# Kernel tuning notes

Measured on AMD Instinct MI355X. Metric: run time of the kernel, lower is better.

## Reference

```python
import jax, jax.numpy as jnp
import numpy as np

B, M, D, HK = 1024, 40, 64, 128

def setup_inputs() -> dict:
    key = jax.random.key(0)
    k1, k2, k3, k4 = jax.random.split(key, 4)
    scale0 = (2.0 / (M + HK)) ** 0.5  # glorot-ish
    scale = (2.0 / (HK + HK)) ** 0.5
    return {
        "x": jax.random.normal(k1, (B, M, D), dtype=jnp.float32),
        "W0": jax.random.normal(k2, (M, M, HK), dtype=jnp.float32) * scale0,
        "W1": jax.random.normal(k3, (M, HK, HK), dtype=jnp.float32) * scale,
        "W2": jax.random.normal(k4, (M, HK, HK), dtype=jnp.float32) * scale,
    }

def reference(x, W0, W1, W2):
    # x: [B, m, D]; layer i: x_next[b,h,d] = sum_{i,j} x0[b,i,d]*xk[b,j,d]*W[i,j,h]
    x0 = x
    xk = x
    outs = []
    for W in (W0, W1, W2):
        # pairwise field interactions per embedding dim: [B, D, m, Hprev]
        z = jnp.einsum('bid,bjd->bdij', x0, xk)
        # contract over both field axes with the filter: [B, Hk, D]
        xk = jnp.einsum('bdij,ijh->bhd', z, W)
        # sum-pool over embedding dim: [B, Hk]
        outs.append(jnp.sum(xk, axis=2))
    return jnp.concatenate(outs, axis=1)  # [B, Hk*k]
```

## Files before the change

### kernel.cpp

```cpp
#include <hip/hip_runtime.h>
#include <cstdint>
#include <cstddef>


typedef __attribute__((ext_vector_type(4))) float f4v;
typedef __attribute__((ext_vector_type(8))) short s8v;

__device__ __forceinline__ unsigned short f2bf(float f){
  unsigned u = __float_as_uint(f);
  u += 0x7fffu + ((u >> 16) & 1u);
  return (unsigned short)(u >> 16);
}

__global__ void prep_weights(const float* __restrict__ W0,
                             const float* __restrict__ W1,
                             const float* __restrict__ W2,
                             unsigned short* __restrict__ ws)
{
  const int total = 327680 + 655360 + 655360;
  for (int e = blockIdx.x * blockDim.x + threadIdx.x; e < total;
       e += gridDim.x * blockDim.x){
    float w; int hi, lo;
    if (e < 327680){
      int h = e / 2560, k = e % 2560;
      int i = k >> 6, j = k & 63;
      w = (j < 40) ? W0[(i*40 + j)*128 + h] : 0.f;
      hi = e; lo = 327680 + e;
    } else if (e < 983040){
      int r = e - 327680;
      int h = r / 5120, k = r % 5120;
      w = W1[k*128 + h];
      hi = 655360 + r; lo = 1310720 + r;
    } else {
      int r = e - 983040;
      int h = r / 5120, k = r % 5120;
      w = W2[k*128 + h];
      hi = 1966080 + r; lo = 2621440 + r;
    }
    unsigned short hb = f2bf(w);
    float whf = __uint_as_float((unsigned)hb << 16);
    unsigned short lb = f2bf(w - whf);
    ws[hi] = hb; ws[lo] = lb;
  }
}


template<int J, int KT>
__device__ __forceinline__ void run_layer(
    const unsigned short* __restrict__ Whi,
    const unsigned short* __restrict__ Wlo,
    const float* __restrict__ xg,
    float* xk, float* __restrict__ out,
    int layerOff, int blockRow, int tid)
{
  const int lane = tid & 63;
  const int wv   = tid >> 6;
  const int cgi  = wv & 1, rgi = wv >> 1;
  const int lrow = lane & 15, q = lane >> 4;

  f4v acc[4][4];
#pragma unroll
  for (int a = 0; a < 4; a++)
#pragma unroll
    for (int b = 0; b < 4; b++)
      acc[a][b] = (f4v){0.f, 0.f, 0.f, 0.f};

  const unsigned short* wp[4];
  const unsigned short* wq[4];
#pragma unroll
  for (int nt = 0; nt < 4; nt++){
    int col = cgi*64 + nt*16 + lrow;
    wp[nt] = Whi + (size_t)col * KT + q*8;
    wq[nt] = Wlo + (size_t)col * KT + q*8;
  }

#pragma unroll 1
  for (int i = 0; i < 40; i++){
    float x0[4];
#pragma unroll
    for (int rt = 0; rt < 4; rt++){
      int gr = blockRow + rgi*64 + rt*16 + lrow;
      x0[rt] = xg[((gr >> 6)*40 + i)*64 + (gr & 63)];
    }
#pragma unroll
    for (int jb = 0; jb < J/32; jb++){
      const int k0 = i*J + jb*32;
      s8v bh[4], bl[4];
#pragma unroll
      for (int nt = 0; nt < 4; nt++){
        bh[nt] = *(const s8v*)(wp[nt] + k0);
        bl[nt] = *(const s8v*)(wq[nt] + k0);
      }
#pragma unroll
      for (int rt = 0; rt < 4; rt++){
        int row = rgi*64 + rt*16 + lrow;
        int w0 = row*128 + ((jb*32 + q*8) ^ ((row & 7) << 2));
        f4v v0 = *(const f4v*)(xk + w0);
        f4v v1 = *(const f4v*)(xk + (w0 ^ 4));
        float s = x0[rt];
        float a0 = s*v0[0], a1 = s*v0[1], a2 = s*v0[2], a3 = s*v0[3];
        float a4 = s*v1[0], a5 = s*v1[1], a6 = s*v1[2], a7 = s*v1[3];
        unsigned ah01, ah23, ah45, ah67, al01, al23, al45, al67;
        asm("v_cvt_pk_bf16_f32 %0, %1, %2" : "=v"(ah01) : "v"(a0), "v"(a1));
        asm("v_cvt_pk_bf16_f32 %0, %1, %2" : "=v"(ah23) : "v"(a2), "v"(a3));
        asm("v_cvt_pk_bf16_f32 %0, %1, %2" : "=v"(ah45) : "v"(a4), "v"(a5));
        asm("v_cvt_pk_bf16_f32 %0, %1, %2" : "=v"(ah67) : "v"(a6), "v"(a7));
        float r0 = a0 - __uint_as_float(ah01 << 16);
        float r1 = a1 - __uint_as_float(ah01 & 0xffff0000u);
        float r2 = a2 - __uint_as_float(ah23 << 16);
        float r3 = a3 - __uint_as_float(ah23 & 0xffff0000u);
        float r4 = a4 - __uint_as_float(ah45 << 16);
        float r5 = a5 - __uint_as_float(ah45 & 0xffff0000u);
        float r6 = a6 - __uint_as_float(ah67 << 16);
        float r7 = a7 - __uint_as_float(ah67 & 0xffff0000u);
        asm("v_cvt_pk_bf16_f32 %0, %1, %2" : "=v"(al01) : "v"(r0), "v"(r1));
        asm("v_cvt_pk_bf16_f32 %0, %1, %2" : "=v"(al23) : "v"(r2), "v"(r3));
        asm("v_cvt_pk_bf16_f32 %0, %1, %2" : "=v"(al45) : "v"(r4), "v"(r5));
        asm("v_cvt_pk_bf16_f32 %0, %1, %2" : "=v"(al67) : "v"(r6), "v"(r7));
        union { unsigned u[4]; s8v v; } Ah, Al;
        Ah.u[0]=ah01; Ah.u[1]=ah23; Ah.u[2]=ah45; Ah.u[3]=ah67;
        Al.u[0]=al01; Al.u[1]=al23; Al.u[2]=al45; Al.u[3]=al67;
#pragma unroll
        for (int nt = 0; nt < 4; nt++){
          acc[rt][nt] = __builtin_amdgcn_mfma_f32_16x16x32_bf16(Ah.v, bh[nt], acc[rt][nt], 0, 0, 0);
          acc[rt][nt] = __builtin_amdgcn_mfma_f32_16x16x32_bf16(Ah.v, bl[nt], acc[rt][nt], 0, 0, 0);
          acc[rt][nt] = __builtin_amdgcn_mfma_f32_16x16x32_bf16(Al.v, bh[nt], acc[rt][nt], 0, 0, 0);
        }
      }
    }
  }
  __syncthreads();
#pragma unroll
  for (int rt = 0; rt < 4; rt++){
#pragma unroll
    for (int nt = 0; nt < 4; nt++){
      int col = cgi*64 + nt*16 + lrow;
#pragma unroll
      for (int r = 0; r < 4; r++){
        int row = rgi*64 + rt*16 + q*4 + r;
        xk[row*128 + (col ^ ((row & 7) << 2))] = acc[rt][nt][r];
      }
    }
  }
  __syncthreads();
  {
    int b_l = tid >> 7, h = tid & 127;
    float sum = 0.f;
#pragma unroll 8
    for (int d = 0; d < 64; d++){
      int row = b_l*64 + d;
      sum += xk[row*128 + (h ^ ((row & 7) << 2))];
    }
    out[(size_t)(blockRow/64 + b_l)*384 + layerOff + h] = sum;
  }
}

__global__ __launch_bounds__(512, 2) void cin_main(
    const float* __restrict__ xg,
    const unsigned short* __restrict__ wsbase,
    float* __restrict__ out)
{
  extern __shared__ float xk[];
  const int tid = threadIdx.x;
  const int blockRow = blockIdx.x * 256;

#pragma unroll 1
  for (int it = 0; it < 32; it++){
    int idx = it*512 + tid;
    int row = idx & 255, j = idx >> 8;
    int gr = blockRow + row;
    float v = 0.f;
    if (j < 40) v = xg[((gr >> 6)*40 + j)*64 + (gr & 63)];
    xk[row*128 + (j ^ ((row & 7) << 2))] = v;
  }
  __syncthreads();

  run_layer< 64, 2560>(wsbase,           wsbase + 327680,  xg, xk, out,   0, blockRow, tid);
  run_layer<128, 5120>(wsbase + 655360,  wsbase + 1310720, xg, xk, out, 128, blockRow, tid);
  run_layer<128, 5120>(wsbase + 1966080, wsbase + 2621440, xg, xk, out, 256, blockRow, tid);
}

extern "C" void kernel_launch(void* const* d_in, const int* in_sizes, int n_in,
                              void* d_out, int out_size, void* d_ws, size_t ws_size,
                              hipStream_t stream)
{
  (void)in_sizes; (void)n_in; (void)out_size; (void)ws_size;
  const float* x  = (const float*)d_in[0];
  const float* W0 = (const float*)d_in[1];
  const float* W1 = (const float*)d_in[2];
  const float* W2 = (const float*)d_in[3];
  float* out = (float*)d_out;
  unsigned short* ws = (unsigned short*)d_ws;

  hipFuncSetAttribute((const void*)cin_main,
                      hipFuncAttributeMaxDynamicSharedMemorySize, 131072);

  prep_weights<<<2048, 256, 0, stream>>>(W0, W1, W2, ws);
  cin_main<<<256, 512, 131072, stream>>>(x, ws, out);
}
```

Baseline: 805.4 us.

## Factor x0 out of the j-contraction and keep xk pre-split as bf16 in LDS

Because x0[b,i,d] does not depend on j, each field i now gets its own MFMA partial t = xk·W_i, which is then scaled by x0 in fp32 and added into the accumulator. The per-element x0*xk product and its bf16 hi/lo split are no longer recomputed inside the inner loop. xk is stored in LDS already split into bf16 hi/lo halves, written once per layer, and the LDS swizzle changes to match. The sum-pool now uses register reductions and wave shuffles instead of a pass through LDS, and the last layer skips its xk writeback. The cost is more register pressure from the extra per-i temporary accumulators, plus a small change in rounding order.

```diff
diff --git a/kernel.cpp b/kernel.cpp
--- a/kernel.cpp
+++ b/kernel.cpp
@@ -45,113 +45,118 @@
 }
 
 
-template<int J, int KT>
+template<int J, int KT, bool WB>
 __device__ __forceinline__ void run_layer(
     const unsigned short* __restrict__ Whi,
-    const unsigned short* __restrict__ Wlo,
     const float* __restrict__ xg,
-    float* xk, float* __restrict__ out,
+    unsigned short* xkU, float* __restrict__ out,
     int layerOff, int blockRow, int tid)
 {
+  constexpr int NJB = J / 32;
+  constexpr size_t WLO = (size_t)128 * KT;
   const int lane = tid & 63;
   const int wv   = tid >> 6;
   const int cgi  = wv & 1, rgi = wv >> 1;
   const int lrow = lane & 15, q = lane >> 4;
 
-  f4v acc[4][4];
+  f4v y[4][4];
 #pragma unroll
   for (int a = 0; a < 4; a++)
 #pragma unroll
-    for (int b = 0; b < 4; b++)
-      acc[a][b] = (f4v){0.f, 0.f, 0.f, 0.f};
+    for (int c = 0; c < 4; c++)
+      y[a][c] = (f4v){0.f, 0.f, 0.f, 0.f};
 
   const unsigned short* wp[4];
-  const unsigned short* wq[4];
-#pragma unroll
-  for (int nt = 0; nt < 4; nt++){
-    int col = cgi*64 + nt*16 + lrow;
-    wp[nt] = Whi + (size_t)col * KT + q*8;
-    wq[nt] = Wlo + (size_t)col * KT + q*8;
-  }
+#pragma unroll
+  for (int nt = 0; nt < 4; nt++)
+    wp[nt] = Whi + (size_t)(cgi*64 + nt*16 + lrow) * KT + q*8;
+
+  const int b = (blockRow >> 6) + rgi;
+  const float* xrow = xg + (size_t)b * 40 * 64;
+  const f4v zero4 = (f4v){0.f, 0.f, 0.f, 0.f};
 
 #pragma unroll 1
   for (int i = 0; i < 40; i++){
-    float x0[4];
-#pragma unroll
-    for (int rt = 0; rt < 4; rt++){
-      int gr = blockRow + rgi*64 + rt*16 + lrow;
-      x0[rt] = xg[((gr >> 6)*40 + i)*64 + (gr & 63)];
-    }
-#pragma unroll
-    for (int jb = 0; jb < J/32; jb++){
+    f4v x0s[4];
+#pragma unroll
+    for (int rt = 0; rt < 4; rt++)
+      x0s[rt] = *(const f4v*)(xrow + i*64 + rt*16 + q*4);
+
+    f4v t[4][4];
+#pragma unroll
+    for (int jb = 0; jb < NJB; jb++){
       const int k0 = i*J + jb*32;
       s8v bh[4], bl[4];
 #pragma unroll
       for (int nt = 0; nt < 4; nt++){
         bh[nt] = *(const s8v*)(wp[nt] + k0);
-        bl[nt] = *(const s8v*)(wq[nt] + k0);
+        bl[nt] = *(const s8v*)(wp[nt] + WLO + k0);
       }
 #pragma unroll
       for (int rt = 0; rt < 4; rt++){
-        int row = rgi*64 + rt*16 + lrow;
-        int w0 = row*128 + ((jb*32 + q*8) ^ ((row & 7) << 2));
-        f4v v0 = *(const f4v*)(xk + w0);
-        f4v v1 = *(const f4v*)(xk + (w0 ^ 4));
-        float s = x0[rt];
-        float a0 = s*v0[0], a1 = s*v0[1], a2 = s*v0[2], a3 = s*v0[3];
-        float a4 = s*v1[0], a5 = s*v1[1], a6 = s*v1[2], a7 = s*v1[3];
-        unsigned ah01, ah23, ah45, ah67, al01, al23, al45, al67;
-        asm("v_cvt_pk_bf16_f32 %0, %1, %2" : "=v"(ah01) : "v"(a0), "v"(a1));
-        asm("v_cvt_pk_bf16_f32 %0, %1, %2" : "=v"(ah23) : "v"(a2), "v"(a3));
-        asm("v_cvt_pk_bf16_f32 %0, %1, %2" : "=v"(ah45) : "v"(a4), "v"(a5));
-        asm("v_cvt_pk_bf16_f32 %0, %1, %2" : "=v"(ah67) : "v"(a6), "v"(a7));
-        float r0 = a0 - __uint_as_float(ah01 << 16);
-        float r1 = a1 - __uint_as_float(ah01 & 0xffff0000u);
-        float r2 = a2 - __uint_as_float(ah23 << 16);
-        float r3 = a3 - __uint_as_float(ah23 & 0xffff0000u);
-        float r4 = a4 - __uint_as_float(ah45 << 16);
-        float r5 = a5 - __uint_as_float(ah45 & 0xffff0000u);
-        float r6 = a6 - __uint_as_float(ah67 << 16);
-        float r7 = a7 - __uint_as_float(ah67 & 0xffff0000u);
-        asm("v_cvt_pk_bf16_f32 %0, %1, %2" : "=v"(al01) : "v"(r0), "v"(r1));
-        asm("v_cvt_pk_bf16_f32 %0, %1, %2" : "=v"(al23) : "v"(r2), "v"(r3));
-        asm("v_cvt_pk_bf16_f32 %0, %1, %2" : "=v"(al45) : "v"(r4), "v"(r5));
-        asm("v_cvt_pk_bf16_f32 %0, %1, %2" : "=v"(al67) : "v"(r6), "v"(r7));
-        union { unsigned u[4]; s8v v; } Ah, Al;
-        Ah.u[0]=ah01; Ah.u[1]=ah23; Ah.u[2]=ah45; Ah.u[3]=ah67;
-        Al.u[0]=al01; Al.u[1]=al23; Al.u[2]=al45; Al.u[3]=al67;
+        const int row = rgi*64 + rt*16 + lrow;
+        const int ci  = row*128 + ((jb*32 + q*8) ^ ((lrow & 7) << 3));
+        const s8v ah = *(const s8v*)(xkU + ci);
+        const s8v al = *(const s8v*)(xkU + 32768 + ci);
 #pragma unroll
         for (int nt = 0; nt < 4; nt++){
-          acc[rt][nt] = __builtin_amdgcn_mfma_f32_16x16x32_bf16(Ah.v, bh[nt], acc[rt][nt], 0, 0, 0);
-          acc[rt][nt] = __builtin_amdgcn_mfma_f32_16x16x32_bf16(Ah.v, bl[nt], acc[rt][nt], 0, 0, 0);
-          acc[rt][nt] = __builtin_amdgcn_mfma_f32_16x16x32_bf16(Al.v, bh[nt], acc[rt][nt], 0, 0, 0);
+          if (jb == 0)
+            t[rt][nt] = __builtin_amdgcn_mfma_f32_16x16x32_bf16(ah, bh[nt], zero4, 0, 0, 0);
+          else
+            t[rt][nt] = __builtin_amdgcn_mfma_f32_16x16x32_bf16(ah, bh[nt], t[rt][nt], 0, 0, 0);
+          t[rt][nt] = __builtin_amdgcn_mfma_f32_16x16x32_bf16(ah, bl[nt], t[rt][nt], 0, 0, 0);
+          t[rt][nt] = __builtin_amdgcn_mfma_f32_16x16x32_bf16(al, bh[nt], t[rt][nt], 0, 0, 0);
         }
       }
     }
-  }
+#pragma unroll
+    for (int rt = 0; rt < 4; rt++)
+#pragma unroll
+      for (int nt = 0; nt < 4; nt++)
+#pragma unroll
+        for (int r = 0; r < 4; r++)
+          y[rt][nt][r] += x0s[rt][r] * t[rt][nt][r];
+  }
+
+  float ps[4];
+#pragma unroll
+  for (int nt = 0; nt < 4; nt++){
+    float s = 0.f;
+#pragma unroll
+    for (int rt = 0; rt < 4; rt++)
+#pragma unroll
+      for (int r = 0; r < 4; r++)
+        s += y[rt][nt][r];
+    s += __shfl_xor(s, 16);
+    s += __shfl_xor(s, 32);
+    ps[nt] = s;
+  }
+  if (q == 0){
+#pragma unroll
+    for (int nt = 0; nt < 4; nt++)
+      out[(size_t)b*384 + layerOff + cgi*64 + nt*16 + lrow] = ps[nt];
+  }
+
   __syncthreads();
-#pragma unroll
-  for (int rt = 0; rt < 4; rt++){
-#pragma unroll
-    for (int nt = 0; nt < 4; nt++){
-      int col = cgi*64 + nt*16 + lrow;
-#pragma unroll
-      for (int r = 0; r < 4; r++){
-        int row = rgi*64 + rt*16 + q*4 + r;
-        xk[row*128 + (col ^ ((row & 7) << 2))] = acc[rt][nt][r];
+  if (WB){
+#pragma unroll
+    for (int rt = 0; rt < 4; rt++){
+#pragma unroll
+      for (int nt = 0; nt < 4; nt++){
+        const int col = cgi*64 + nt*16 + lrow;
+#pragma unroll
+        for (int r = 0; r < 4; r++){
+          const int row = rgi*64 + rt*16 + q*4 + r;
+          const float v = y[rt][nt][r];
+          unsigned short hb = f2bf(v);
+          unsigned short lb = f2bf(v - __uint_as_float((unsigned)hb << 16));
+          const int pi = row*128 + (col ^ ((row & 7) << 3));
+          xkU[pi] = hb;
+          xkU[32768 + pi] = lb;
+        }
       }
     }
-  }
-  __syncthreads();
-  {
-    int b_l = tid >> 7, h = tid & 127;
-    float sum = 0.f;
-#pragma unroll 8
-    for (int d = 0; d < 64; d++){
-      int row = b_l*64 + d;
-      sum += xk[row*128 + (h ^ ((row & 7) << 2))];
-    }
-    out[(size_t)(blockRow/64 + b_l)*384 + layerOff + h] = sum;
+    __syncthreads();
   }
 }
 
@@ -160,7 +165,7 @@
     const unsigned short* __restrict__ wsbase,
     float* __restrict__ out)
 {
-  extern __shared__ float xk[];
+  extern __shared__ unsigned short xkU[];
   const int tid = threadIdx.x;
   const int blockRow = blockIdx.x * 256;
 
@@ -168,16 +173,22 @@
   for (int it = 0; it < 32; it++){
     int idx = it*512 + tid;
     int row = idx & 255, j = idx >> 8;
-    int gr = blockRow + row;
     float v = 0.f;
-    if (j < 40) v = xg[((gr >> 6)*40 + j)*64 + (gr & 63)];
-    xk[row*128 + (j ^ ((row & 7) << 2))] = v;
+    if (j < 40){
+      int bb = (blockRow >> 6) + (row >> 6);
+      v = xg[((size_t)bb*40 + j)*64 + (row & 63)];
+    }
+    unsigned short hb = f2bf(v);
+    unsigned short lb = f2bf(v - __uint_as_float((unsigned)hb << 16));
+    const int pi = row*128 + (j ^ ((row & 7) << 3));
+    xkU[pi] = hb;
+    xkU[32768 + pi] = lb;
   }
   __syncthreads();
 
-  run_layer< 64, 2560>(wsbase,           wsbase + 327680,  xg, xk, out,   0, blockRow, tid);
-  run_layer<128, 5120>(wsbase + 655360,  wsbase + 1310720, xg, xk, out, 128, blockRow, tid);
-  run_layer<128, 5120>(wsbase + 1966080, wsbase + 2621440, xg, xk, out, 256, blockRow, tid);
+  run_layer< 64, 2560, true >(wsbase,           xg, xkU, out,   0, blockRow, tid);
+  run_layer<128, 5120, true >(wsbase + 655360,  xg, xkU, out, 128, blockRow, tid);
+  run_layer<128, 5120, false>(wsbase + 1966080, xg, xkU, out, 256, blockRow, tid);
 }
 
 extern "C" void kernel_launch(void* const* d_in, const int* in_sizes, int n_in,
```

After: 1.260 ms. 1.56x slower.
